# Kernel tuning notes

Measured on AMD Instinct MI355X. Metric: run time of the kernel, lower is better.

Reference implementation:

```python
import jax, jax.numpy as jnp
import numpy as np

HEADS = 16

def setup_inputs() -> dict:
    key = jax.random.key(0)
    ks = jax.random.split(key, 6)
    b, n, d, k = 4, 4096, 1024, 256
    return {
        "x": jax.random.normal(ks[0], (b, n, d), dtype=jnp.float32),
        "Wq": jax.random.normal(ks[1], (d, d), dtype=jnp.float32) * 0.02,
        "Wk": jax.random.normal(ks[2], (d, d), dtype=jnp.float32) * 0.02,
        "Wv": jax.random.normal(ks[3], (d, d), dtype=jnp.float32) * 0.02,
        "proj_k": jax.random.normal(ks[4], (n, k), dtype=jnp.float32) * 0.02,
        "proj_v": jax.random.normal(ks[5], (n, k), dtype=jnp.float32) * 0.02,
    }

def reference(x, Wq, Wk, Wv, proj_k, proj_v):
    b, n, d = x.shape
    h = HEADS
    dh = d // h
    k = proj_k.shape[1]
    # Q/K/V projections (no bias)
    q = jnp.einsum('bnd,de->bne', x, Wq)          # [b,n,d]
    keys = jnp.einsum('bnd,de->bne', x, Wk)       # [b,n,d]
    vals = jnp.einsum('bnd,de->bne', x, Wv)       # [b,n,d]
    # low-rank sequence projection: n -> k
    keys = jnp.einsum('bnd,nk->bkd', keys, proj_k)   # [b,k,d]
    vals = jnp.einsum('bnd,nk->bkd', vals, proj_v)   # [b,k,d]
    # split heads
    q = q.reshape(b, n, h, dh).transpose(0, 2, 1, 3)      # [b,h,n,dh]
    keys = keys.reshape(b, k, h, dh).transpose(0, 2, 1, 3)  # [b,h,k,dh]
    vals = vals.reshape(b, k, h, dh).transpose(0, 2, 1, 3)  # [b,h,k,dh]
    # attention over reduced k dim (NOTE: module applies no 1/sqrt(dh) scale)
    dots = jnp.einsum('bhnd,bhkd->bhnk', q, keys)
    attn = jax.nn.softmax(dots, axis=-1)
    out = jnp.einsum('bhnk,bhkd->bhnd', attn, vals)
    return out.transpose(0, 2, 1, 3).reshape(b, n, d)
```

## Files before the change

### kernel.cpp

```cpp
#include <hip/hip_runtime.h>


typedef __fp16 f16x8 __attribute__((ext_vector_type(8)));
typedef __fp16 f16x2 __attribute__((ext_vector_type(2)));
typedef float fl4 __attribute__((ext_vector_type(4)));
typedef float f32x4 __attribute__((ext_vector_type(4)));
typedef unsigned int u32x2 __attribute__((ext_vector_type(2)));
typedef unsigned int u32x4 __attribute__((ext_vector_type(4)));

#define MFMA16(a, b, c) __builtin_amdgcn_mfma_f32_16x16x32_f16((a), (b), (c), 0, 0, 0)

__device__ __forceinline__ unsigned int pk2u(float a, float b) {
  f16x2 p = __builtin_amdgcn_cvt_pkrtz(a, b);
  return __builtin_bit_cast(unsigned int, p);
}

__device__ __forceinline__ f16x8 pk8(fl4 a, fl4 b) {
  f16x2 p0 = __builtin_amdgcn_cvt_pkrtz(a[0], a[1]);
  f16x2 p1 = __builtin_amdgcn_cvt_pkrtz(a[2], a[3]);
  f16x2 p2 = __builtin_amdgcn_cvt_pkrtz(b[0], b[1]);
  f16x2 p3 = __builtin_amdgcn_cvt_pkrtz(b[2], b[3]);
  f16x8 r;
  r[0] = p0[0]; r[1] = p0[1]; r[2] = p1[0]; r[3] = p1[1];
  r[4] = p2[0]; r[5] = p2[1]; r[6] = p3[0]; r[7] = p3[1];
  return r;
}

__device__ __forceinline__ void gload_lds16(const __fp16* g, void* lds_base) {
  __builtin_amdgcn_global_load_lds(
      (const __attribute__((address_space(1))) void*)g,
      (__attribute__((address_space(3))) void*)lds_base, 16, 0, 0);
}

__device__ __forceinline__ f16x8 rd_swz(const __fp16* base, int row, int lg) {
  return *(const f16x8*)((const char*)base + row * 64 +
                         ((lg ^ ((row >> 1) & 3)) * 16));
}

__device__ __forceinline__ f16x8 rd128(const __fp16* base, int row, int ch) {
  return *(const f16x8*)((const char*)base + row * 128 +
                         ((ch ^ (row & 7)) * 16));
}

__global__ __launch_bounds__(256) void tr_cvt(
    const float* __restrict__ in, __fp16* __restrict__ out, int R, int C) {
  __shared__ float tile[32][33];
  const int t = threadIdx.x;
  const int c0 = blockIdx.x * 32, r0 = blockIdx.y * 32;
  {
    const int r = t >> 3, cg = (t & 7) * 4;
    fl4 v = *(const fl4*)(in + (size_t)(r0 + r) * C + c0 + cg);
    tile[r][cg] = v[0]; tile[r][cg + 1] = v[1];
    tile[r][cg + 2] = v[2]; tile[r][cg + 3] = v[3];
  }
  __syncthreads();
  {
    const int cc = t >> 3, rg = (t & 7) * 4;
    u32x2 p;
    p[0] = pk2u(tile[rg + 0][cc], tile[rg + 1][cc]);
    p[1] = pk2u(tile[rg + 2][cc], tile[rg + 3][cc]);
    *(u32x2*)(out + (size_t)(c0 + cc) * R + r0 + rg) = p;
  }
}

__global__ __launch_bounds__(256) void xprep(
    const float* __restrict__ X, __fp16* __restrict__ Xf,
    __fp16* __restrict__ XT) {
  __shared__ float tile[32][65];
  const int t = threadIdx.x;
  const int n0 = blockIdx.x * 32, d0 = blockIdx.y * 64, b = blockIdx.z;
  const float* src = X + ((size_t)b * 4096 + n0) * 1024 + d0;
  {
    const int r = t >> 3, cg = (t & 7) * 8;
    fl4 v0 = *(const fl4*)(src + (size_t)r * 1024 + cg);
    fl4 v1 = *(const fl4*)(src + (size_t)r * 1024 + cg + 4);
    *(f16x8*)(Xf + ((size_t)b * 4096 + n0 + r) * 1024 + d0 + cg) = pk8(v0, v1);
#pragma unroll
    for (int j = 0; j < 4; ++j) {
      tile[r][cg + j] = v0[j];
      tile[r][cg + 4 + j] = v1[j];
    }
  }
  __syncthreads();
  {
    const int d = t >> 2, ng = (t & 3) * 8;
    fl4 a, c;
#pragma unroll
    for (int j = 0; j < 4; ++j) {
      a[j] = tile[ng + j][d];
      c[j] = tile[ng + 4 + j][d];
    }
    *(f16x8*)(XT + ((size_t)b * 1024 + d0 + d) * 4096 + n0 + ng) = pk8(a, c);
  }
}

__global__ __launch_bounds__(256) void stage1_partial(
    const __fp16* __restrict__ pkT,
    const __fp16* __restrict__ pvT,
    const __fp16* __restrict__ XT,
    float* __restrict__ Pk,
    float* __restrict__ Pv) {
  __shared__ __fp16 Ak[64 * 64];
  __shared__ __fp16 Av[64 * 64];
  __shared__ __fp16 Bx[64 * 64];
  const int t = threadIdx.x;
  const int lane = t & 63, w = t >> 6;
  const int lr = lane & 15, lg = lane >> 4;
  const int fid = blockIdx.x;
  const int g = fid >> 5, s5 = fid & 31;
  const int kk0 = (s5 >> 3) * 64, p8 = s5 & 7;
  const int pr = g * 8 + p8;
  const int dd0 = (pr & 15) * 64;
  const int z = pr >> 4, b = z & 3, c = z >> 2;
  const int wr = (w >> 1) * 32, wc = (w & 1) * 32;

  f32x4 acck[2][2], accv[2][2];
#pragma unroll
  for (int i = 0; i < 2; ++i)
#pragma unroll
    for (int j = 0; j < 2; ++j) {
      acck[i][j] = (f32x4){0.f, 0.f, 0.f, 0.f};
      accv[i][j] = (f32x4){0.f, 0.f, 0.f, 0.f};
    }

  const int r8 = lane >> 3, c8 = lane & 7;
  const int ssw = ((c8 ^ r8) * 8);
  const __fp16* pkS0 = pkT + (size_t)(kk0 + w * 8 + r8) * 4096 + c * 1024 + ssw;
  const __fp16* pkS1 = pkS0 + (size_t)32 * 4096;
  const __fp16* pvS0 = pvT + (size_t)(kk0 + w * 8 + r8) * 4096 + c * 1024 + ssw;
  const __fp16* pvS1 = pvS0 + (size_t)32 * 4096;
  const __fp16* xS0 =
      XT + ((size_t)b * 1024 + dd0 + w * 8 + r8) * 4096 + c * 1024 + ssw;
  const __fp16* xS1 = xS0 + (size_t)32 * 4096;

  for (int it = 0; it < 16; ++it) {
    const int n0 = it * 64;
    __syncthreads();
    gload_lds16(pkS0 + n0, (char*)Ak + w * 1024);
    gload_lds16(pkS1 + n0, (char*)Ak + 4096 + w * 1024);
    gload_lds16(pvS0 + n0, (char*)Av + w * 1024);
    gload_lds16(pvS1 + n0, (char*)Av + 4096 + w * 1024);
    gload_lds16(xS0 + n0, (char*)Bx + w * 1024);
    gload_lds16(xS1 + n0, (char*)Bx + 4096 + w * 1024);
    __syncthreads();

#pragma unroll
    for (int s = 0; s < 2; ++s) {
      f16x8 ak[2], av[2], bx[2];
#pragma unroll
      for (int i = 0; i < 2; ++i) {
        ak[i] = rd128(Ak, wr + i * 16 + lr, s * 4 + lg);
        av[i] = rd128(Av, wr + i * 16 + lr, s * 4 + lg);
      }
#pragma unroll
      for (int j = 0; j < 2; ++j)
        bx[j] = rd128(Bx, wc + j * 16 + lr, s * 4 + lg);
#pragma unroll
      for (int i = 0; i < 2; ++i)
#pragma unroll
        for (int j = 0; j < 2; ++j) {
          acck[i][j] = MFMA16(ak[i], bx[j], acck[i][j]);
          accv[i][j] = MFMA16(av[i], bx[j], accv[i][j]);
        }
    }
  }

#pragma unroll
  for (int i = 0; i < 2; ++i)
#pragma unroll
    for (int j = 0; j < 2; ++j)
#pragma unroll
      for (int r = 0; r < 4; ++r) {
        const size_t row = (size_t)z * 256 + kk0 + wr + i * 16 + lg * 4 + r;
        const int col = dd0 + wc + j * 16 + lr;
        Pk[row * 1024 + col] = acck[i][j][r];
        Pv[row * 1024 + col] = accv[i][j][r];
      }
}

__global__ __launch_bounds__(256) void stage1_reduce(
    const float* __restrict__ Pk, const float* __restrict__ Pv,
    __fp16* __restrict__ Xk, __fp16* __restrict__ Xv) {
  const size_t base = ((size_t)blockIdx.x * 256 + threadIdx.x) * 4;
  const int b = (int)(base >> 18);
  const size_t rem = base & 0x3FFFFu;
  fl4 ak = (fl4){0.f, 0.f, 0.f, 0.f}, av = (fl4){0.f, 0.f, 0.f, 0.f};
#pragma unroll
  for (int c = 0; c < 4; ++c) {
    const size_t off = (((size_t)(c * 4 + b)) << 18) + rem;
    ak += *(const fl4*)(Pk + off);
    av += *(const fl4*)(Pv + off);
  }
  u32x2 pkp, pvp;
  pkp[0] = pk2u(ak[0], ak[1]); pkp[1] = pk2u(ak[2], ak[3]);
  pvp[0] = pk2u(av[0], av[1]); pvp[1] = pk2u(av[2], av[3]);
  *(u32x2*)(Xk + base) = pkp;
  *(u32x2*)(Xv + base) = pvp;
}

__global__ __launch_bounds__(256) void bt64(
    const __fp16* __restrict__ A, long long bsA,
    const __fp16* __restrict__ B, long long bsB,
    __fp16* __restrict__ C, int ldC, long long bsC) {
  constexpr int E = 1024;
  __shared__ __fp16 As[64 * 32];
  __shared__ __fp16 Bs[64 * 32];
  const int t = threadIdx.x;
  const int lane = t & 63, w = t >> 6;
  const int lr = lane & 15, lg = lane >> 4;
  const int i0 = blockIdx.x * 64, j0 = blockIdx.y * 64;
  A += (size_t)blockIdx.z * (size_t)bsA;
  B += (size_t)blockIdx.z * (size_t)bsB;
  C += (size_t)blockIdx.z * (size_t)bsC;
  const int wr = (w >> 1) * 32, wc = (w & 1) * 32;

  f32x4 acc[2][2];
#pragma unroll
  for (int i = 0; i < 2; ++i)
#pragma unroll
    for (int j = 0; j < 2; ++j) acc[i][j] = (f32x4){0.f, 0.f, 0.f, 0.f};

  const int gl_row = w * 16 + (lane >> 2);
  const int gl_ch = (lane & 3) ^ ((lane >> 3) & 3);
  const __fp16* aSrc = A + (size_t)(i0 + gl_row) * E + gl_ch * 8;
  const __fp16* bSrc = B + (size_t)(j0 + gl_row) * E + gl_ch * 8;

  for (int e0 = 0; e0 < E; e0 += 32) {
    __syncthreads();
    gload_lds16(aSrc + e0, (char*)As + w * 1024);
    gload_lds16(bSrc + e0, (char*)Bs + w * 1024);
    __syncthreads();

    f16x8 af[2], bf[2];
#pragma unroll
    for (int i = 0; i < 2; ++i)
      af[i] = rd_swz(As, wr + i * 16 + lr, lg);
#pragma unroll
    for (int j = 0; j < 2; ++j)
      bf[j] = rd_swz(Bs, wc + j * 16 + lr, lg);
#pragma unroll
    for (int i = 0; i < 2; ++i)
#pragma unroll
      for (int j = 0; j < 2; ++j)
        acc[i][j] = MFMA16(af[i], bf[j], acc[i][j]);
  }

#pragma unroll
  for (int i = 0; i < 2; ++i)
#pragma unroll
    for (int j = 0; j < 2; ++j)
#pragma unroll
      for (int r = 0; r < 4; ++r) {
        const int row = i0 + wr + i * 16 + lg * 4 + r;
        const int col = j0 + wc + j * 16 + lr;
        C[(size_t)row * ldC + col] = (__fp16)acc[i][j][r];
      }
}

__global__ __launch_bounds__(256) void gemm_q(
    const __fp16* __restrict__ Xf,
    const __fp16* __restrict__ WT,
    __fp16* __restrict__ Q) {
  constexpr int K = 1024, N = 1024;
  __shared__ __fp16 Xs[128 * 64];
  __shared__ __fp16 Ws[128 * 64];
  const int t = threadIdx.x;
  const int lane = t & 63, w = t >> 6;
  const int lr = lane & 15, lg = lane >> 4;
  const int fid = blockIdx.x;
  const int g = fid >> 6, s6 = fid & 63;
  const int n0 = (s6 >> 3) * 128;
  const int m0 = (g * 8 + (s6 & 7)) * 128;
  const int wr = (w >> 1) * 64, wc = (w & 1) * 64;

  f32x4 acc[4][4];
#pragma unroll
  for (int i = 0; i < 4; ++i)
#pragma unroll
    for (int j = 0; j < 4; ++j) acc[i][j] = (f32x4){0.f, 0.f, 0.f, 0.f};

  const int r8 = lane >> 3, c8 = lane & 7;
  const int ssw = ((c8 ^ r8) * 8);
  const __fp16* xS = Xf + (size_t)(m0 + w * 8 + r8) * K + ssw;
  const __fp16* wS = WT + (size_t)(n0 + w * 8 + r8) * K + ssw;

  for (int it = 0; it < 16; ++it) {
    const int k0 = it * 64;
    __syncthreads();
#pragma unroll
    for (int i = 0; i < 4; ++i) {
      gload_lds16(xS + (size_t)i * 32 * K + k0, (char*)Xs + i * 4096 + w * 1024);
      gload_lds16(wS + (size_t)i * 32 * K + k0, (char*)Ws + i * 4096 + w * 1024);
    }
    __syncthreads();

#pragma unroll
    for (int s = 0; s < 2; ++s) {
      f16x8 af[4], bf[4];
#pragma unroll
      for (int i = 0; i < 4; ++i)
        af[i] = rd128(Xs, wr + i * 16 + lr, s * 4 + lg);
#pragma unroll
      for (int j = 0; j < 4; ++j)
        bf[j] = rd128(Ws, wc + j * 16 + lr, s * 4 + lg);
#pragma unroll
      for (int i = 0; i < 4; ++i)
#pragma unroll
        for (int j = 0; j < 4; ++j)
          acc[i][j] = MFMA16(af[i], bf[j], acc[i][j]);
    }
  }

#pragma unroll
  for (int i = 0; i < 4; ++i)
#pragma unroll
    for (int j = 0; j < 4; ++j)
#pragma unroll
      for (int r = 0; r < 4; ++r) {
        const int row = m0 + wr + i * 16 + lg * 4 + r;
        const int col = n0 + wc + j * 16 + lr;
        Q[(size_t)row * N + col] = (__fp16)acc[i][j][r];
      }
}

__global__ __launch_bounds__(256) void attn_k(
    const __fp16* __restrict__ Q,
    const __fp16* __restrict__ Kp,
    const __fp16* __restrict__ Vpt,
    float* __restrict__ O) {
  __shared__ __fp16 KV[256 * 64];
  const int t = threadIdx.x;
  const int lane = t & 63, w = t >> 6;
  const int lr = lane & 15, lg = lane >> 4;
  const int bh = blockIdx.x >> 5, rb = blockIdx.x & 31;
  const int b = bh >> 4, h = bh & 15;
  const int m0 = rb * 128 + w * 32;

  const __fp16* Kph = Kp + (size_t)b * 256 * 1024 + h * 64;
  const __fp16* Vph = Vpt + ((size_t)b * 1024 + h * 64) * 256;
  const __fp16* Qh = Q + ((size_t)(b * 4096 + m0)) * 1024 + h * 64;

#pragma unroll
  for (int i = 0; i < 8; ++i) {
    const int kr = (i * 4 + w) * 8 + (lane >> 3);
    gload_lds16(Kph + (size_t)kr * 1024 + (((lane & 7) ^ (kr & 7)) * 8),
                (char*)KV + (i * 4 + w) * 1024);
  }

  f16x8 aq[2][2];
#pragma unroll
  for (int mi = 0; mi < 2; ++mi)
#pragma unroll
    for (int s = 0; s < 2; ++s)
      aq[mi][s] =
          *(const f16x8*)(Qh + (size_t)(mi * 16 + lr) * 1024 + s * 32 + lg * 8);

  __syncthreads();

  f32x4 dots[2][16];
#pragma unroll
  for (int mi = 0; mi < 2; ++mi)
#pragma unroll
    for (int jt = 0; jt < 16; ++jt) dots[mi][jt] = (f32x4){0.f, 0.f, 0.f, 0.f};
#pragma unroll
  for (int jt = 0; jt < 16; ++jt) {
    const int r = jt * 16 + lr;
    f16x8 k0 = *(const f16x8*)((const char*)KV + r * 128 + ((lg ^ (r & 7)) * 16));
    f16x8 k1 =
        *(const f16x8*)((const char*)KV + r * 128 + (((4 + lg) ^ (r & 7)) * 16));
    dots[0][jt] = MFMA16(k0, aq[0][0], dots[0][jt]);
    dots[0][jt] = MFMA16(k1, aq[0][1], dots[0][jt]);
    dots[1][jt] = MFMA16(k0, aq[1][0], dots[1][jt]);
    dots[1][jt] = MFMA16(k1, aq[1][1], dots[1][jt]);
  }

  unsigned cpk[2][16][2];
  float smv[2];
#pragma unroll
  for (int mi = 0; mi < 2; ++mi) {
    float mx = -1e30f;
#pragma unroll
    for (int jt = 0; jt < 16; ++jt)
#pragma unroll
      for (int r = 0; r < 4; ++r) mx = fmaxf(mx, dots[mi][jt][r]);
    mx = fmaxf(mx, __shfl_xor(mx, 16, 64));
    mx = fmaxf(mx, __shfl_xor(mx, 32, 64));
    float sm = 0.f;
#pragma unroll
    for (int jt = 0; jt < 16; ++jt) {
#pragma unroll
      for (int r = 0; r < 4; ++r) {
        float p = __expf(dots[mi][jt][r] - mx);
        dots[mi][jt][r] = p;
        sm += p;
      }
      cpk[mi][jt][0] = pk2u(dots[mi][jt][0], dots[mi][jt][1]);
      cpk[mi][jt][1] = pk2u(dots[mi][jt][2], dots[mi][jt][3]);
    }
    sm += __shfl_xor(sm, 16, 64);
    sm += __shfl_xor(sm, 32, 64);
    smv[mi] = sm;
  }

  __syncthreads();

#pragma unroll
  for (int i = 0; i < 8; ++i) {
    const int dd = (i * 4 + w) * 2 + (lane >> 5);
    gload_lds16(Vph + (size_t)dd * 256 + (((lane & 31) ^ (dd & 7)) * 8),
                (char*)KV + (i * 4 + w) * 1024);
  }
  __syncthreads();

#pragma unroll
  for (int mi = 0; mi < 2; ++mi) {
    f32x4 o[4];
#pragma unroll
    for (int j = 0; j < 4; ++j) o[j] = (f32x4){0.f, 0.f, 0.f, 0.f};
#pragma unroll
    for (int ks = 0; ks < 8; ++ks) {
      u32x4 wds;
#pragma unroll
      for (int m = 0; m < 4; ++m) {
        const int addr = ((((lane & 16) >> 3) + (m >> 1)) * 16 + lr) * 4;
        const int a0 = __builtin_amdgcn_ds_bpermute(
            addr, (int)cpk[mi][ks * 2][m & 1]);
        const int a1 = __builtin_amdgcn_ds_bpermute(
            addr, (int)cpk[mi][ks * 2 + 1][m & 1]);
        wds[m] = (unsigned)((lg >> 1) ? a1 : a0);
      }
      f16x8 pa = __builtin_bit_cast(f16x8, wds);
#pragma unroll
      for (int jt2 = 0; jt2 < 4; ++jt2) {
        const int dd = jt2 * 16 + lr;
        f16x8 bv = *(const f16x8*)((const char*)KV + dd * 512 +
                                   (((ks * 4 + lg) ^ (dd & 7)) * 16));
        o[jt2] = MFMA16(pa, bv, o[jt2]);
      }
    }

    float rs[4];
#pragma unroll
    for (int r = 0; r < 4; ++r)
      rs[r] = 1.f / __shfl(smv[mi], (lane & 48) + lg * 4 + r, 64);
#pragma unroll
    for (int jt2 = 0; jt2 < 4; ++jt2)
#pragma unroll
      for (int r = 0; r < 4; ++r) {
        const size_t row = (size_t)(b * 4096 + m0 + mi * 16 + lg * 4 + r);
        O[row * 1024 + h * 64 + jt2 * 16 + lr] = o[jt2][r] * rs[r];
      }
  }
}

extern "C" void kernel_launch(void* const* d_in, const int* in_sizes, int n_in,
                              void* d_out, int out_size, void* d_ws, size_t ws_size,
                              hipStream_t stream) {
  (void)in_sizes; (void)n_in; (void)out_size; (void)ws_size;
  const float* x  = (const float*)d_in[0];
  const float* Wq = (const float*)d_in[1];
  const float* Wk = (const float*)d_in[2];
  const float* Wv = (const float*)d_in[3];
  const float* pk = (const float*)d_in[4];
  const float* pv = (const float*)d_in[5];
  float* out = (float*)d_out;

  __fp16* Qh  = (__fp16*)d_ws;
  __fp16* WqT = Qh  + (size_t)16384 * 1024;
  __fp16* WkT = WqT + (size_t)1024 * 1024;
  __fp16* WvT = WkT + (size_t)1024 * 1024;
  __fp16* pkT = WvT + (size_t)1024 * 1024;
  __fp16* pvT = pkT + (size_t)256 * 4096;
  __fp16* Xk  = pvT + (size_t)256 * 4096;
  __fp16* Xv  = Xk  + (size_t)4 * 256 * 1024;
  __fp16* Kp  = Xv  + (size_t)4 * 256 * 1024;
  __fp16* Vpt = Kp  + (size_t)4 * 256 * 1024;
  float* Pk = (float*)d_ws;
  float* Pv = Pk + (size_t)16 * 256 * 1024;
  __fp16* Xf16 = (__fp16*)d_out;
  __fp16* XT   = Xf16 + (size_t)4 * 4096 * 1024;

  const dim3 bb(256);

  xprep<<<dim3(128, 16, 4), bb, 0, stream>>>(x, Xf16, XT);
  tr_cvt<<<dim3(32, 32), bb, 0, stream>>>(Wq, WqT, 1024, 1024);
  tr_cvt<<<dim3(32, 32), bb, 0, stream>>>(Wk, WkT, 1024, 1024);
  tr_cvt<<<dim3(32, 32), bb, 0, stream>>>(Wv, WvT, 1024, 1024);
  tr_cvt<<<dim3(8, 128), bb, 0, stream>>>(pk, pkT, 4096, 256);
  tr_cvt<<<dim3(8, 128), bb, 0, stream>>>(pv, pvT, 4096, 256);

  stage1_partial<<<dim3(1024), bb, 0, stream>>>(pkT, pvT, XT, Pk, Pv);
  stage1_reduce<<<dim3(1024), bb, 0, stream>>>(Pk, Pv, Xk, Xv);

  bt64<<<dim3(4, 16, 4), bb, 0, stream>>>(Xk, 256LL * 1024, WkT, 0LL,
                                          Kp, 1024, 256LL * 1024);
  bt64<<<dim3(16, 4, 4), bb, 0, stream>>>(WvT, 0LL, Xv, 256LL * 1024,
                                          Vpt, 256, 1024LL * 256);

  gemm_q<<<dim3(1024), bb, 0, stream>>>(Xf16, WqT, Qh);

  attn_k<<<dim3(2048), bb, 0, stream>>>(Qh, Kp, Vpt, out);
}
```

Before: 189.2 us.

## Fuse Q projection GEMM into attention kernel and drop Q round-trip

Removes the separate gemm_q kernel and computes each block's 128x64 Q tile inside the attention kernel, staging it through shared memory instead of writing and rereading a full fp16 Q tensor in global memory. Workspace buffers are rearranged so Xf16 lives in the workspace and XT/Pk/Pv in the output buffer. Block indices are swizzled so blocks sharing the same head's Wq slice run close together. The cost is a smaller per-block GEMM tile (128x64 instead of 128x128), so X is reloaded 16 times across heads, which raises L2/HBM traffic.

```diff
diff --git a/kernel.cpp b/kernel.cpp
--- a/kernel.cpp
+++ b/kernel.cpp
@@ -257,74 +257,9 @@
       }
 }
 
-__global__ __launch_bounds__(256) void gemm_q(
+__global__ __launch_bounds__(256) void attn_fused(
     const __fp16* __restrict__ Xf,
-    const __fp16* __restrict__ WT,
-    __fp16* __restrict__ Q) {
-  constexpr int K = 1024, N = 1024;
-  __shared__ __fp16 Xs[128 * 64];
-  __shared__ __fp16 Ws[128 * 64];
-  const int t = threadIdx.x;
-  const int lane = t & 63, w = t >> 6;
-  const int lr = lane & 15, lg = lane >> 4;
-  const int fid = blockIdx.x;
-  const int g = fid >> 6, s6 = fid & 63;
-  const int n0 = (s6 >> 3) * 128;
-  const int m0 = (g * 8 + (s6 & 7)) * 128;
-  const int wr = (w >> 1) * 64, wc = (w & 1) * 64;
-
-  f32x4 acc[4][4];
-#pragma unroll
-  for (int i = 0; i < 4; ++i)
-#pragma unroll
-    for (int j = 0; j < 4; ++j) acc[i][j] = (f32x4){0.f, 0.f, 0.f, 0.f};
-
-  const int r8 = lane >> 3, c8 = lane & 7;
-  const int ssw = ((c8 ^ r8) * 8);
-  const __fp16* xS = Xf + (size_t)(m0 + w * 8 + r8) * K + ssw;
-  const __fp16* wS = WT + (size_t)(n0 + w * 8 + r8) * K + ssw;
-
-  for (int it = 0; it < 16; ++it) {
-    const int k0 = it * 64;
-    __syncthreads();
-#pragma unroll
-    for (int i = 0; i < 4; ++i) {
-      gload_lds16(xS + (size_t)i * 32 * K + k0, (char*)Xs + i * 4096 + w * 1024);
-      gload_lds16(wS + (size_t)i * 32 * K + k0, (char*)Ws + i * 4096 + w * 1024);
-    }
-    __syncthreads();
-
-#pragma unroll
-    for (int s = 0; s < 2; ++s) {
-      f16x8 af[4], bf[4];
-#pragma unroll
-      for (int i = 0; i < 4; ++i)
-        af[i] = rd128(Xs, wr + i * 16 + lr, s * 4 + lg);
-#pragma unroll
-      for (int j = 0; j < 4; ++j)
-        bf[j] = rd128(Ws, wc + j * 16 + lr, s * 4 + lg);
-#pragma unroll
-      for (int i = 0; i < 4; ++i)
-#pragma unroll
-        for (int j = 0; j < 4; ++j)
-          acc[i][j] = MFMA16(af[i], bf[j], acc[i][j]);
-    }
-  }
-
-#pragma unroll
-  for (int i = 0; i < 4; ++i)
-#pragma unroll
-    for (int j = 0; j < 4; ++j)
-#pragma unroll
-      for (int r = 0; r < 4; ++r) {
-        const int row = m0 + wr + i * 16 + lg * 4 + r;
-        const int col = n0 + wc + j * 16 + lr;
-        Q[(size_t)row * N + col] = (__fp16)acc[i][j][r];
-      }
-}
-
-__global__ __launch_bounds__(256) void attn_k(
-    const __fp16* __restrict__ Q,
+    const __fp16* __restrict__ WqT,
     const __fp16* __restrict__ Kp,
     const __fp16* __restrict__ Vpt,
     float* __restrict__ O) {
@@ -332,13 +267,82 @@
   const int t = threadIdx.x;
   const int lane = t & 63, w = t >> 6;
   const int lr = lane & 15, lg = lane >> 4;
-  const int bh = blockIdx.x >> 5, rb = blockIdx.x & 31;
-  const int b = bh >> 4, h = bh & 15;
+  const int fid = blockIdx.x;
+  const int orig = (fid & 7) * 256 + (fid >> 3);
+  const int h = orig & 15;
+  const int rb = (orig >> 4) & 31;
+  const int b = orig >> 9;
   const int m0 = rb * 128 + w * 32;
+
+  const int r8 = lane >> 3, c8 = lane & 7;
+  const int ssw = (c8 ^ r8) * 8;
+
+  __fp16* Xs = KV;
+  __fp16* Ws = KV + 8192;
+  const __fp16* xS = Xf + ((size_t)(b * 4096 + rb * 128) + w * 8 + r8) * 1024 + ssw;
+  const __fp16* wS = WqT + (size_t)(h * 64 + w * 8 + r8) * 1024 + ssw;
+
+  f32x4 qacc[2][4];
+#pragma unroll
+  for (int i = 0; i < 2; ++i)
+#pragma unroll
+    for (int j = 0; j < 4; ++j) qacc[i][j] = (f32x4){0.f, 0.f, 0.f, 0.f};
+
+  for (int it = 0; it < 16; ++it) {
+    const int k0 = it * 64;
+    __syncthreads();
+#pragma unroll
+    for (int i = 0; i < 4; ++i)
+      gload_lds16(xS + (size_t)i * 32 * 1024 + k0, (char*)Xs + i * 4096 + w * 1024);
+#pragma unroll
+    for (int i = 0; i < 2; ++i)
+      gload_lds16(wS + (size_t)i * 32 * 1024 + k0, (char*)Ws + i * 4096 + w * 1024);
+    __syncthreads();
+
+#pragma unroll
+    for (int s = 0; s < 2; ++s) {
+      f16x8 af[2], bf[4];
+#pragma unroll
+      for (int mi = 0; mi < 2; ++mi)
+        af[mi] = rd128(Xs, w * 32 + mi * 16 + lr, s * 4 + lg);
+#pragma unroll
+      for (int jj = 0; jj < 4; ++jj)
+        bf[jj] = rd128(Ws, jj * 16 + lr, s * 4 + lg);
+#pragma unroll
+      for (int mi = 0; mi < 2; ++mi)
+#pragma unroll
+        for (int jj = 0; jj < 4; ++jj)
+          qacc[mi][jj] = MFMA16(af[mi], bf[jj], qacc[mi][jj]);
+    }
+  }
+  __syncthreads();
+
+  {
+    char* Qs = (char*)KV;
+#pragma unroll
+    for (int mi = 0; mi < 2; ++mi)
+#pragma unroll
+      for (int jj = 0; jj < 4; ++jj)
+#pragma unroll
+        for (int r = 0; r < 4; ++r) {
+          const int row = w * 32 + mi * 16 + lg * 4 + r;
+          const int e = jj * 16 + lr;
+          *(__fp16*)(Qs + row * 128 + (((e >> 3) ^ (row & 7)) * 16) +
+                     (e & 7) * 2) = (__fp16)qacc[mi][jj][r];
+        }
+  }
+  __syncthreads();
+
+  f16x8 aq[2][2];
+#pragma unroll
+  for (int mi = 0; mi < 2; ++mi)
+#pragma unroll
+    for (int s = 0; s < 2; ++s)
+      aq[mi][s] = rd128(KV, w * 32 + mi * 16 + lr, s * 4 + lg);
+  __syncthreads();
 
   const __fp16* Kph = Kp + (size_t)b * 256 * 1024 + h * 64;
   const __fp16* Vph = Vpt + ((size_t)b * 1024 + h * 64) * 256;
-  const __fp16* Qh = Q + ((size_t)(b * 4096 + m0)) * 1024 + h * 64;
 
 #pragma unroll
   for (int i = 0; i < 8; ++i) {
@@ -346,15 +350,6 @@
     gload_lds16(Kph + (size_t)kr * 1024 + (((lane & 7) ^ (kr & 7)) * 8),
                 (char*)KV + (i * 4 + w) * 1024);
   }
-
-  f16x8 aq[2][2];
-#pragma unroll
-  for (int mi = 0; mi < 2; ++mi)
-#pragma unroll
-    for (int s = 0; s < 2; ++s)
-      aq[mi][s] =
-          *(const f16x8*)(Qh + (size_t)(mi * 16 + lr) * 1024 + s * 32 + lg * 8);
-
   __syncthreads();
 
   f32x4 dots[2][16];
@@ -465,8 +460,8 @@
   const float* pv = (const float*)d_in[5];
   float* out = (float*)d_out;
 
-  __fp16* Qh  = (__fp16*)d_ws;
-  __fp16* WqT = Qh  + (size_t)16384 * 1024;
+  __fp16* Xf16 = (__fp16*)d_ws;
+  __fp16* WqT = Xf16 + (size_t)16384 * 1024;
   __fp16* WkT = WqT + (size_t)1024 * 1024;
   __fp16* WvT = WkT + (size_t)1024 * 1024;
   __fp16* pkT = WvT + (size_t)1024 * 1024;
@@ -475,10 +470,9 @@
   __fp16* Xv  = Xk  + (size_t)4 * 256 * 1024;
   __fp16* Kp  = Xv  + (size_t)4 * 256 * 1024;
   __fp16* Vpt = Kp  + (size_t)4 * 256 * 1024;
-  float* Pk = (float*)d_ws;
+  __fp16* XT = (__fp16*)d_out;
+  float* Pk = (float*)(XT + (size_t)4 * 1024 * 4096);
   float* Pv = Pk + (size_t)16 * 256 * 1024;
-  __fp16* Xf16 = (__fp16*)d_out;
-  __fp16* XT   = Xf16 + (size_t)4 * 4096 * 1024;
 
   const dim3 bb(256);
 
@@ -497,7 +491,5 @@
   bt64<<<dim3(16, 4, 4), bb, 0, stream>>>(WvT, 0LL, Xv, 256LL * 1024,
                                           Vpt, 256, 1024LL * 256);
 
-  gemm_q<<<dim3(1024), bb, 0, stream>>>(Xf16, WqT, Qh);
-
-  attn_k<<<dim3(2048), bb, 0, stream>>>(Qh, Kp, Vpt, out);
-}
+  attn_fused<<<dim3(2048), bb, 0, stream>>>(Xf16, WqT, Kp, Vpt, out);
+}
```

Result: slower. 248.6 us (+31.4%).

## Double-buffer LDS tiles in stage1, bt64 and gemm_q GEMM loops

Applied to the files above, without the earlier changes.

Gives the stage1_partial, bt64 and gemm_q kernels two LDS buffers, so the global-to-LDS loads for the next K step are issued while MFMAs run on the current step. This hides load latency and removes one barrier per iteration. gemm_q also drops its K step from 64 to 32 and switches to the 32-wide swizzled layout, keeping its LDS footprint the same but doubling its iteration count. The risk is that gload_lds16 needs no explicit wait before the single trailing barrier; if the compiler does not insert a vmcnt wait there, the next step could read incomplete data. stage1 also doubles its LDS use, which can lower occupancy.

```diff
diff --git a/kernel.cpp b/kernel.cpp
--- a/kernel.cpp
+++ b/kernel.cpp
@@ -100,9 +100,9 @@
     const __fp16* __restrict__ XT,
     float* __restrict__ Pk,
     float* __restrict__ Pv) {
-  __shared__ __fp16 Ak[64 * 64];
-  __shared__ __fp16 Av[64 * 64];
-  __shared__ __fp16 Bx[64 * 64];
+  __shared__ __fp16 Ak[2][64 * 64];
+  __shared__ __fp16 Av[2][64 * 64];
+  __shared__ __fp16 Bx[2][64 * 64];
   const int t = threadIdx.x;
   const int lane = t & 63, w = t >> 6;
   const int lr = lane & 15, lg = lane >> 4;
@@ -133,28 +133,36 @@
       XT + ((size_t)b * 1024 + dd0 + w * 8 + r8) * 4096 + c * 1024 + ssw;
   const __fp16* xS1 = xS0 + (size_t)32 * 4096;
 
+  gload_lds16(pkS0, (char*)Ak[0] + w * 1024);
+  gload_lds16(pkS1, (char*)Ak[0] + 4096 + w * 1024);
+  gload_lds16(pvS0, (char*)Av[0] + w * 1024);
+  gload_lds16(pvS1, (char*)Av[0] + 4096 + w * 1024);
+  gload_lds16(xS0, (char*)Bx[0] + w * 1024);
+  gload_lds16(xS1, (char*)Bx[0] + 4096 + w * 1024);
+  __syncthreads();
+
   for (int it = 0; it < 16; ++it) {
-    const int n0 = it * 64;
-    __syncthreads();
-    gload_lds16(pkS0 + n0, (char*)Ak + w * 1024);
-    gload_lds16(pkS1 + n0, (char*)Ak + 4096 + w * 1024);
-    gload_lds16(pvS0 + n0, (char*)Av + w * 1024);
-    gload_lds16(pvS1 + n0, (char*)Av + 4096 + w * 1024);
-    gload_lds16(xS0 + n0, (char*)Bx + w * 1024);
-    gload_lds16(xS1 + n0, (char*)Bx + 4096 + w * 1024);
-    __syncthreads();
-
+    const int cur = it & 1, nxt = cur ^ 1;
+    if (it < 15) {
+      const int n1 = (it + 1) * 64;
+      gload_lds16(pkS0 + n1, (char*)Ak[nxt] + w * 1024);
+      gload_lds16(pkS1 + n1, (char*)Ak[nxt] + 4096 + w * 1024);
+      gload_lds16(pvS0 + n1, (char*)Av[nxt] + w * 1024);
+      gload_lds16(pvS1 + n1, (char*)Av[nxt] + 4096 + w * 1024);
+      gload_lds16(xS0 + n1, (char*)Bx[nxt] + w * 1024);
+      gload_lds16(xS1 + n1, (char*)Bx[nxt] + 4096 + w * 1024);
+    }
 #pragma unroll
     for (int s = 0; s < 2; ++s) {
       f16x8 ak[2], av[2], bx[2];
 #pragma unroll
       for (int i = 0; i < 2; ++i) {
-        ak[i] = rd128(Ak, wr + i * 16 + lr, s * 4 + lg);
-        av[i] = rd128(Av, wr + i * 16 + lr, s * 4 + lg);
+        ak[i] = rd128(Ak[cur], wr + i * 16 + lr, s * 4 + lg);
+        av[i] = rd128(Av[cur], wr + i * 16 + lr, s * 4 + lg);
       }
 #pragma unroll
       for (int j = 0; j < 2; ++j)
-        bx[j] = rd128(Bx, wc + j * 16 + lr, s * 4 + lg);
+        bx[j] = rd128(Bx[cur], wc + j * 16 + lr, s * 4 + lg);
 #pragma unroll
       for (int i = 0; i < 2; ++i)
 #pragma unroll
@@ -163,6 +171,7 @@
           accv[i][j] = MFMA16(av[i], bx[j], accv[i][j]);
         }
     }
+    __syncthreads();
   }
 
 #pragma unroll
@@ -203,8 +212,8 @@
     const __fp16* __restrict__ B, long long bsB,
     __fp16* __restrict__ C, int ldC, long long bsC) {
   constexpr int E = 1024;
-  __shared__ __fp16 As[64 * 32];
-  __shared__ __fp16 Bs[64 * 32];
+  __shared__ __fp16 As[2][64 * 32];
+  __shared__ __fp16 Bs[2][64 * 32];
   const int t = threadIdx.x;
   const int lane = t & 63, w = t >> 6;
   const int lr = lane & 15, lg = lane >> 4;
@@ -225,24 +234,30 @@
   const __fp16* aSrc = A + (size_t)(i0 + gl_row) * E + gl_ch * 8;
   const __fp16* bSrc = B + (size_t)(j0 + gl_row) * E + gl_ch * 8;
 
-  for (int e0 = 0; e0 < E; e0 += 32) {
-    __syncthreads();
-    gload_lds16(aSrc + e0, (char*)As + w * 1024);
-    gload_lds16(bSrc + e0, (char*)Bs + w * 1024);
-    __syncthreads();
-
+  gload_lds16(aSrc, (char*)As[0] + w * 1024);
+  gload_lds16(bSrc, (char*)Bs[0] + w * 1024);
+  __syncthreads();
+
+  for (int it = 0; it < 32; ++it) {
+    const int cur = it & 1, nxt = cur ^ 1;
+    if (it < 31) {
+      const int e1 = (it + 1) * 32;
+      gload_lds16(aSrc + e1, (char*)As[nxt] + w * 1024);
+      gload_lds16(bSrc + e1, (char*)Bs[nxt] + w * 1024);
+    }
     f16x8 af[2], bf[2];
 #pragma unroll
     for (int i = 0; i < 2; ++i)
-      af[i] = rd_swz(As, wr + i * 16 + lr, lg);
+      af[i] = rd_swz(As[cur], wr + i * 16 + lr, lg);
 #pragma unroll
     for (int j = 0; j < 2; ++j)
-      bf[j] = rd_swz(Bs, wc + j * 16 + lr, lg);
+      bf[j] = rd_swz(Bs[cur], wc + j * 16 + lr, lg);
 #pragma unroll
     for (int i = 0; i < 2; ++i)
 #pragma unroll
       for (int j = 0; j < 2; ++j)
         acc[i][j] = MFMA16(af[i], bf[j], acc[i][j]);
+    __syncthreads();
   }
 
 #pragma unroll
@@ -262,8 +277,8 @@
     const __fp16* __restrict__ WT,
     __fp16* __restrict__ Q) {
   constexpr int K = 1024, N = 1024;
-  __shared__ __fp16 Xs[128 * 64];
-  __shared__ __fp16 Ws[128 * 64];
+  __shared__ __fp16 Xs[2][128 * 32];
+  __shared__ __fp16 Ws[2][128 * 32];
   const int t = threadIdx.x;
   const int lane = t & 63, w = t >> 6;
   const int lr = lane & 15, lg = lane >> 4;
@@ -279,36 +294,41 @@
 #pragma unroll
     for (int j = 0; j < 4; ++j) acc[i][j] = (f32x4){0.f, 0.f, 0.f, 0.f};
 
-  const int r8 = lane >> 3, c8 = lane & 7;
-  const int ssw = ((c8 ^ r8) * 8);
-  const __fp16* xS = Xf + (size_t)(m0 + w * 8 + r8) * K + ssw;
-  const __fp16* wS = WT + (size_t)(n0 + w * 8 + r8) * K + ssw;
-
-  for (int it = 0; it < 16; ++it) {
-    const int k0 = it * 64;
+  const int gl_row = w * 16 + (lane >> 2);
+  const int gl_ch = (lane & 3) ^ ((lane >> 3) & 3);
+  const __fp16* xS0 = Xf + (size_t)(m0 + gl_row) * K + gl_ch * 8;
+  const __fp16* xS1 = xS0 + (size_t)64 * K;
+  const __fp16* wS0 = WT + (size_t)(n0 + gl_row) * K + gl_ch * 8;
+  const __fp16* wS1 = wS0 + (size_t)64 * K;
+
+  gload_lds16(xS0, (char*)Xs[0] + w * 1024);
+  gload_lds16(xS1, (char*)Xs[0] + 4096 + w * 1024);
+  gload_lds16(wS0, (char*)Ws[0] + w * 1024);
+  gload_lds16(wS1, (char*)Ws[0] + 4096 + w * 1024);
+  __syncthreads();
+
+  for (int it = 0; it < 32; ++it) {
+    const int cur = it & 1, nxt = cur ^ 1;
+    if (it < 31) {
+      const int k1 = (it + 1) * 32;
+      gload_lds16(xS0 + k1, (char*)Xs[nxt] + w * 1024);
+      gload_lds16(xS1 + k1, (char*)Xs[nxt] + 4096 + w * 1024);
+      gload_lds16(wS0 + k1, (char*)Ws[nxt] + w * 1024);
+      gload_lds16(wS1 + k1, (char*)Ws[nxt] + 4096 + w * 1024);
+    }
+    f16x8 af[4], bf[4];
+#pragma unroll
+    for (int i = 0; i < 4; ++i)
+      af[i] = rd_swz(Xs[cur], wr + i * 16 + lr, lg);
+#pragma unroll
+    for (int j = 0; j < 4; ++j)
+      bf[j] = rd_swz(Ws[cur], wc + j * 16 + lr, lg);
+#pragma unroll
+    for (int i = 0; i < 4; ++i)
+#pragma unroll
+      for (int j = 0; j < 4; ++j)
+        acc[i][j] = MFMA16(af[i], bf[j], acc[i][j]);
     __syncthreads();
-#pragma unroll
-    for (int i = 0; i < 4; ++i) {
-      gload_lds16(xS + (size_t)i * 32 * K + k0, (char*)Xs + i * 4096 + w * 1024);
-      gload_lds16(wS + (size_t)i * 32 * K + k0, (char*)Ws + i * 4096 + w * 1024);
-    }
-    __syncthreads();
-
-#pragma unroll
-    for (int s = 0; s < 2; ++s) {
-      f16x8 af[4], bf[4];
-#pragma unroll
-      for (int i = 0; i < 4; ++i)
-        af[i] = rd128(Xs, wr + i * 16 + lr, s * 4 + lg);
-#pragma unroll
-      for (int j = 0; j < 4; ++j)
-        bf[j] = rd128(Ws, wc + j * 16 + lr, s * 4 + lg);
-#pragma unroll
-      for (int i = 0; i < 4; ++i)
-#pragma unroll
-        for (int j = 0; j < 4; ++j)
-          acc[i][j] = MFMA16(af[i], bf[j], acc[i][j]);
-    }
   }
 
 #pragma unroll
```

New measurement: 211.4 us. +11.7%, slower.

## Use 32x32 MFMA tiles in attention and batch weight transpose launches

Applied to the files above, without the earlier changes.

The attention kernel moves from 16x16x32 MFMA tiles to 32x32x16 tiles, so each wave handles its 32 query rows as one tile. Softmax normalisation is folded into the probabilities before packing, and the ds_bpermute relayout becomes a single cross-half shuffle. The five transpose-convert launches are merged into two batched launches using blockIdx.z. The aim is fewer LDS reads and permutes per MFMA and less launch overhead, at the cost of larger accumulator register use and fp16 rounding of already-normalised probabilities.

```diff
diff --git a/kernel.cpp b/kernel.cpp
--- a/kernel.cpp
+++ b/kernel.cpp
@@ -5,10 +5,12 @@
 typedef __fp16 f16x2 __attribute__((ext_vector_type(2)));
 typedef float fl4 __attribute__((ext_vector_type(4)));
 typedef float f32x4 __attribute__((ext_vector_type(4)));
+typedef float f32x16 __attribute__((ext_vector_type(16)));
 typedef unsigned int u32x2 __attribute__((ext_vector_type(2)));
 typedef unsigned int u32x4 __attribute__((ext_vector_type(4)));
 
 #define MFMA16(a, b, c) __builtin_amdgcn_mfma_f32_16x16x32_f16((a), (b), (c), 0, 0, 0)
+#define MFMA32(a, b, c) __builtin_amdgcn_mfma_f32_32x32x16_f16((a), (b), (c), 0, 0, 0)
 
 __device__ __forceinline__ unsigned int pk2u(float a, float b) {
   f16x2 p = __builtin_amdgcn_cvt_pkrtz(a, b);
@@ -42,8 +44,8 @@
                          ((ch ^ (row & 7)) * 16));
 }
 
-__global__ __launch_bounds__(256) void tr_cvt(
-    const float* __restrict__ in, __fp16* __restrict__ out, int R, int C) {
+__device__ __forceinline__ void tr_cvt_body(
+    const float* in, __fp16* out, int R, int C) {
   __shared__ float tile[32][33];
   const int t = threadIdx.x;
   const int c0 = blockIdx.x * 32, r0 = blockIdx.y * 32;
@@ -61,6 +63,23 @@
     p[1] = pk2u(tile[rg + 2][cc], tile[rg + 3][cc]);
     *(u32x2*)(out + (size_t)(c0 + cc) * R + r0 + rg) = p;
   }
+}
+
+__global__ __launch_bounds__(256) void tr_cvt3(
+    const float* __restrict__ i0, const float* __restrict__ i1,
+    const float* __restrict__ i2, __fp16* __restrict__ o0,
+    __fp16* __restrict__ o1, __fp16* __restrict__ o2) {
+  const float* in = (blockIdx.z == 0) ? i0 : (blockIdx.z == 1) ? i1 : i2;
+  __fp16* out = (blockIdx.z == 0) ? o0 : (blockIdx.z == 1) ? o1 : o2;
+  tr_cvt_body(in, out, 1024, 1024);
+}
+
+__global__ __launch_bounds__(256) void tr_cvt2(
+    const float* __restrict__ i0, const float* __restrict__ i1,
+    __fp16* __restrict__ o0, __fp16* __restrict__ o1) {
+  const float* in = (blockIdx.z == 0) ? i0 : i1;
+  __fp16* out = (blockIdx.z == 0) ? o0 : o1;
+  tr_cvt_body(in, out, 4096, 256);
 }
 
 __global__ __launch_bounds__(256) void xprep(
@@ -331,7 +350,7 @@
   __shared__ __fp16 KV[256 * 64];
   const int t = threadIdx.x;
   const int lane = t & 63, w = t >> 6;
-  const int lr = lane & 15, lg = lane >> 4;
+  const int l31 = lane & 31, b5 = lane >> 5;
   const int bh = blockIdx.x >> 5, rb = blockIdx.x & 31;
   const int b = bh >> 4, h = bh & 15;
   const int m0 = rb * 128 + w * 32;
@@ -347,60 +366,60 @@
                 (char*)KV + (i * 4 + w) * 1024);
   }
 
-  f16x8 aq[2][2];
-#pragma unroll
-  for (int mi = 0; mi < 2; ++mi)
-#pragma unroll
-    for (int s = 0; s < 2; ++s)
-      aq[mi][s] =
-          *(const f16x8*)(Qh + (size_t)(mi * 16 + lr) * 1024 + s * 32 + lg * 8);
+  f16x8 bq[4];
+#pragma unroll
+  for (int s = 0; s < 4; ++s)
+    bq[s] = *(const f16x8*)(Qh + (size_t)l31 * 1024 + s * 16 + b5 * 8);
 
   __syncthreads();
 
-  f32x4 dots[2][16];
-#pragma unroll
-  for (int mi = 0; mi < 2; ++mi)
-#pragma unroll
-    for (int jt = 0; jt < 16; ++jt) dots[mi][jt] = (f32x4){0.f, 0.f, 0.f, 0.f};
-#pragma unroll
-  for (int jt = 0; jt < 16; ++jt) {
-    const int r = jt * 16 + lr;
-    f16x8 k0 = *(const f16x8*)((const char*)KV + r * 128 + ((lg ^ (r & 7)) * 16));
-    f16x8 k1 =
-        *(const f16x8*)((const char*)KV + r * 128 + (((4 + lg) ^ (r & 7)) * 16));
-    dots[0][jt] = MFMA16(k0, aq[0][0], dots[0][jt]);
-    dots[0][jt] = MFMA16(k1, aq[0][1], dots[0][jt]);
-    dots[1][jt] = MFMA16(k0, aq[1][0], dots[1][jt]);
-    dots[1][jt] = MFMA16(k1, aq[1][1], dots[1][jt]);
-  }
-
-  unsigned cpk[2][16][2];
-  float smv[2];
-#pragma unroll
-  for (int mi = 0; mi < 2; ++mi) {
-    float mx = -1e30f;
-#pragma unroll
-    for (int jt = 0; jt < 16; ++jt)
-#pragma unroll
-      for (int r = 0; r < 4; ++r) mx = fmaxf(mx, dots[mi][jt][r]);
-    mx = fmaxf(mx, __shfl_xor(mx, 16, 64));
-    mx = fmaxf(mx, __shfl_xor(mx, 32, 64));
-    float sm = 0.f;
-#pragma unroll
-    for (int jt = 0; jt < 16; ++jt) {
-#pragma unroll
-      for (int r = 0; r < 4; ++r) {
-        float p = __expf(dots[mi][jt][r] - mx);
-        dots[mi][jt][r] = p;
-        sm += p;
-      }
-      cpk[mi][jt][0] = pk2u(dots[mi][jt][0], dots[mi][jt][1]);
-      cpk[mi][jt][1] = pk2u(dots[mi][jt][2], dots[mi][jt][3]);
-    }
-    sm += __shfl_xor(sm, 16, 64);
-    sm += __shfl_xor(sm, 32, 64);
-    smv[mi] = sm;
-  }
+  f32x16 dots[8];
+#pragma unroll
+  for (int tile = 0; tile < 8; ++tile) {
+    f32x16 d = {};
+#pragma unroll
+    for (int s = 0; s < 4; ++s) {
+      f16x8 ka = rd128(KV, tile * 32 + l31, s * 2 + b5);
+      d = MFMA32(ka, bq[s], d);
+    }
+    dots[tile] = d;
+  }
+
+  float mx = -1e30f;
+#pragma unroll
+  for (int tile = 0; tile < 8; ++tile)
+#pragma unroll
+    for (int r = 0; r < 16; ++r) mx = fmaxf(mx, dots[tile][r]);
+  mx = fmaxf(mx, __shfl_xor(mx, 32, 64));
+  float sm = 0.f;
+#pragma unroll
+  for (int tile = 0; tile < 8; ++tile)
+#pragma unroll
+    for (int r = 0; r < 16; ++r) {
+      float p = __expf(dots[tile][r] - mx);
+      dots[tile][r] = p;
+      sm += p;
+    }
+  sm += __shfl_xor(sm, 32, 64);
+  const float rs = 1.f / sm;
+
+  unsigned pkw[8][8];
+#pragma unroll
+  for (int tile = 0; tile < 8; ++tile)
+#pragma unroll
+    for (int half = 0; half < 2; ++half) {
+      const int rb8 = half * 8;
+      const unsigned A0 = pk2u(dots[tile][rb8 + 0] * rs, dots[tile][rb8 + 1] * rs);
+      const unsigned A1 = pk2u(dots[tile][rb8 + 2] * rs, dots[tile][rb8 + 3] * rs);
+      const unsigned B0 = pk2u(dots[tile][rb8 + 4] * rs, dots[tile][rb8 + 5] * rs);
+      const unsigned B1 = pk2u(dots[tile][rb8 + 6] * rs, dots[tile][rb8 + 7] * rs);
+      const unsigned s0 = __shfl_xor(b5 ? A0 : B0, 32, 64);
+      const unsigned s1 = __shfl_xor(b5 ? A1 : B1, 32, 64);
+      pkw[tile][half * 4 + 0] = b5 ? s0 : A0;
+      pkw[tile][half * 4 + 1] = b5 ? s1 : A1;
+      pkw[tile][half * 4 + 2] = b5 ? B0 : s0;
+      pkw[tile][half * 4 + 3] = b5 ? B1 : s1;
+    }
 
   __syncthreads();
 
@@ -412,45 +431,35 @@
   }
   __syncthreads();
 
-#pragma unroll
-  for (int mi = 0; mi < 2; ++mi) {
-    f32x4 o[4];
-#pragma unroll
-    for (int j = 0; j < 4; ++j) o[j] = (f32x4){0.f, 0.f, 0.f, 0.f};
-#pragma unroll
-    for (int ks = 0; ks < 8; ++ks) {
+  f32x16 o[2];
+  o[0] = (f32x16){};
+  o[1] = (f32x16){};
+#pragma unroll
+  for (int tile = 0; tile < 8; ++tile)
+#pragma unroll
+    for (int half = 0; half < 2; ++half) {
       u32x4 wds;
 #pragma unroll
-      for (int m = 0; m < 4; ++m) {
-        const int addr = ((((lane & 16) >> 3) + (m >> 1)) * 16 + lr) * 4;
-        const int a0 = __builtin_amdgcn_ds_bpermute(
-            addr, (int)cpk[mi][ks * 2][m & 1]);
-        const int a1 = __builtin_amdgcn_ds_bpermute(
-            addr, (int)cpk[mi][ks * 2 + 1][m & 1]);
-        wds[m] = (unsigned)((lg >> 1) ? a1 : a0);
+      for (int m = 0; m < 4; ++m) wds[m] = pkw[tile][half * 4 + m];
+      f16x8 pa = __builtin_bit_cast(f16x8, wds);
+      const int ks = tile * 2 + half;
+#pragma unroll
+      for (int dt = 0; dt < 2; ++dt) {
+        const int dd = dt * 32 + l31;
+        f16x8 bv = *(const f16x8*)(
+            (const char*)KV + dd * 512 + (((ks * 2 + b5) ^ (dd & 7)) * 16));
+        o[dt] = MFMA32(pa, bv, o[dt]);
       }
-      f16x8 pa = __builtin_bit_cast(f16x8, wds);
-#pragma unroll
-      for (int jt2 = 0; jt2 < 4; ++jt2) {
-        const int dd = jt2 * 16 + lr;
-        f16x8 bv = *(const f16x8*)((const char*)KV + dd * 512 +
-                                   (((ks * 4 + lg) ^ (dd & 7)) * 16));
-        o[jt2] = MFMA16(pa, bv, o[jt2]);
-      }
-    }
-
-    float rs[4];
-#pragma unroll
-    for (int r = 0; r < 4; ++r)
-      rs[r] = 1.f / __shfl(smv[mi], (lane & 48) + lg * 4 + r, 64);
-#pragma unroll
-    for (int jt2 = 0; jt2 < 4; ++jt2)
-#pragma unroll
-      for (int r = 0; r < 4; ++r) {
-        const size_t row = (size_t)(b * 4096 + m0 + mi * 16 + lg * 4 + r);
-        O[row * 1024 + h * 64 + jt2 * 16 + lr] = o[jt2][r] * rs[r];
-      }
-  }
+    }
+
+#pragma unroll
+  for (int dt = 0; dt < 2; ++dt)
+#pragma unroll
+    for (int r = 0; r < 16; ++r) {
+      const int q = (r & 3) + 8 * (r >> 2) + 4 * b5;
+      const size_t row = (size_t)(b * 4096 + m0 + q);
+      O[row * 1024 + h * 64 + dt * 32 + l31] = o[dt][r];
+    }
 }
 
 extern "C" void kernel_launch(void* const* d_in, const int* in_sizes, int n_in,
@@ -483,11 +492,8 @@
   const dim3 bb(256);
 
   xprep<<<dim3(128, 16, 4), bb, 0, stream>>>(x, Xf16, XT);
-  tr_cvt<<<dim3(32, 32), bb, 0, stream>>>(Wq, WqT, 1024, 1024);
-  tr_cvt<<<dim3(32, 32), bb, 0, stream>>>(Wk, WkT, 1024, 1024);
-  tr_cvt<<<dim3(32, 32), bb, 0, stream>>>(Wv, WvT, 1024, 1024);
-  tr_cvt<<<dim3(8, 128), bb, 0, stream>>>(pk, pkT, 4096, 256);
-  tr_cvt<<<dim3(8, 128), bb, 0, stream>>>(pv, pvT, 4096, 256);
+  tr_cvt3<<<dim3(32, 32, 3), bb, 0, stream>>>(Wq, Wk, Wv, WqT, WkT, WvT);
+  tr_cvt2<<<dim3(8, 128, 2), bb, 0, stream>>>(pk, pv, pkT, pvT);
 
   stage1_partial<<<dim3(1024), bb, 0, stream>>>(pkT, pvT, XT, Pk, Pv);
   stage1_reduce<<<dim3(1024), bb, 0, stream>>>(Pk, Pv, Xk, Xv);
```

New measurement: 195.6 us. +3.4%, slower.
